# Kernel tuning notes

Measured on AMD Instinct MI355X. Metric: run time of the kernel, lower is better.

## Reference

```python
import jax, jax.numpy as jnp
import numpy as np

N_NODES = 100000
N_EDGES = 1000000
N_RELS = 8
N_HEADS = 4
IN_FEAT = 64
OUT_FEAT = 64
D_HEAD = OUT_FEAT // N_HEADS
LEAKY_SLOPE = 0.2


def setup_inputs() -> dict:
    key = jax.random.key(0)
    ks = jax.random.split(key, 8)
    x = jax.random.normal(ks[0], (N_NODES, IN_FEAT), dtype=jnp.float32)
    src_idx = jax.random.randint(ks[1], (N_EDGES,), 0, N_NODES)
    dst_idx = jax.random.randint(ks[2], (N_EDGES,), 0, N_NODES)
    edge_rel = jnp.sort(jax.random.randint(ks[3], (N_EDGES,), 0, N_RELS))
    # xavier-ish small init for weights
    conv_weights = jax.random.normal(ks[4], (N_RELS, N_HEADS, IN_FEAT, D_HEAD), dtype=jnp.float32) * 0.1
    attn_l = jax.random.normal(ks[5], (N_RELS, N_HEADS, D_HEAD), dtype=jnp.float32) * 0.1
    attn_r = jax.random.normal(ks[6], (N_RELS, N_HEADS, D_HEAD), dtype=jnp.float32) * 0.1
    h_bias = jnp.zeros((OUT_FEAT,), dtype=jnp.float32)
    return {
        'x': x, 'src_idx': src_idx, 'dst_idx': dst_idx, 'edge_rel': edge_rel,
        'conv_weights': conv_weights, 'attn_l': attn_l, 'attn_r': attn_r,
        'h_bias': h_bias,
    }


def reference(x, src_idx, dst_idx, edge_rel, conv_weights, attn_l, attn_r, h_bias):
    N = x.shape[0]
    # Per-relation transform of all node features: [R, N, H, D]
    feat_all = jnp.einsum('ni,rhid->rnhd', x, conv_weights)
    # Per-relation attention logits per node: [R, N, H]
    el_all = jnp.einsum('rnhd,rhd->rnh', feat_all, attn_l)
    er_all = jnp.einsum('rnhd,rhd->rnh', feat_all, attn_r)
    # Gather per-edge quantities (relation-specific transform of src/dst)
    feat_e = feat_all[edge_rel, src_idx]          # [E, H, D]
    el = el_all[edge_rel, src_idx]                # [E, H]
    er = er_all[edge_rel, dst_idx]                # [E, H]
    s = jax.nn.leaky_relu(el + er, negative_slope=LEAKY_SLOPE)
    # Edge softmax over incoming edges of each destination node (per head)
    m = jax.ops.segment_max(s, dst_idx, num_segments=N)      # [N, H]
    e = jnp.exp(s - m[dst_idx])                               # [E, H]
    denom = jax.ops.segment_sum(e, dst_idx, num_segments=N)   # [N, H]
    w = e / jnp.maximum(denom[dst_idx], jnp.float32(1e-16))   # [E, H]
    # Weighted aggregation of source features into destination nodes
    agg = jax.ops.segment_sum(feat_e * w[..., None], dst_idx, num_segments=N)  # [N, H, D]
    h = agg.reshape(N, OUT_FEAT) + h_bias
    # activation=None, dropout in eval mode -> identity
    return h
```

## Files before the change

### kernel.cpp

```cpp
#include <hip/hip_runtime.h>
#include <hip/hip_bf16.h>

#define NN 100000
#define NE 1000000
#define NR 8

#define EB 4096
#define NBLK 245
#define NBUCK 196
#define NT (NBUCK*NBLK)
#define NBB 188

typedef unsigned short u16;
typedef unsigned int u32;
typedef __attribute__((ext_vector_type(8))) short bf16x8;
typedef __attribute__((ext_vector_type(4))) float f32x4;

static __device__ __forceinline__ float bf2f(u16 u) {
    union { u32 i; float f; } v; v.i = ((u32)u) << 16; return v.f;
}
static __device__ __forceinline__ float bflo(u32 u) {
    union { u32 i; float f; } v; v.i = u << 16; return v.f;
}
static __device__ __forceinline__ float bfhi(u32 u) {
    union { u32 i; float f; } v; v.i = u & 0xffff0000u; return v.f;
}
static __device__ __forceinline__ u16 f2bf(float f) {
    __hip_bfloat16 h = __float2bfloat16(f);
    return *reinterpret_cast<u16*>(&h);
}
static __device__ __forceinline__ float ldf(const void* p, int idx, int isf32) {
    return isf32 ? ((const float*)p)[idx] : bf2f(((const u16*)p)[idx]);
}

__global__ void k_detect(const u16* __restrict__ xw, int* __restrict__ flag)
{
    int t = threadIdx.x;
    int insane = 0;
    for (int k = t; k < 512; k += 64) {
        u16 w = xw[k];
        int ex = (w >> 7) & 0xFF;
        bool sane = ((w & 0x7FFF) == 0) || (ex >= 96 && ex <= 159);
        insane += sane ? 0 : 1;
    }
    for (int off = 32; off; off >>= 1) insane += __shfl_down(insane, off);
    if (t == 0) *flag = (insane > 50) ? 1 : 0;
}

__global__ void k_cvt(const void* __restrict__ xin, const int* __restrict__ flag,
                      u16* __restrict__ xb)
{
    int i = blockIdx.x * blockDim.x + threadIdx.x;
    if (i >= NN * 8) return;
    if (*flag) {
        const float* xf = (const float*)xin;
        u16 o[8];
#pragma unroll
        for (int j = 0; j < 8; ++j) o[j] = f2bf(xf[i * 8 + j]);
        uint4 v;
        v.x = (u32)o[0] | ((u32)o[1] << 16);
        v.y = (u32)o[2] | ((u32)o[3] << 16);
        v.z = (u32)o[4] | ((u32)o[5] << 16);
        v.w = (u32)o[6] | ((u32)o[7] << 16);
        ((uint4*)xb)[i] = v;
    } else {
        ((uint4*)xb)[i] = ((const uint4*)xin)[i];
    }
}

__global__ void k0_prep(const void* __restrict__ cw, const void* __restrict__ al,
                        const void* __restrict__ ar, const int* __restrict__ flag,
                        u16* __restrict__ Bpre)
{
    int tid = blockIdx.x * blockDim.x + threadIdx.x;
    if (tid >= NR * 5120) return;
    int isf32 = *flag;
    int r = tid / 5120, rem = tid % 5120;
    int c = rem >> 3, j = rem & 7;
    int nt = c >> 7, kk = (c >> 6) & 1, lc = c & 63;
    int i = kk * 32 + ((lc >> 4) << 3) + j;
    int d = lc & 15;
    u16 val;
    if (nt < 4) {
        val = f2bf(ldf(cw, ((r * 4 + nt) * 64 + i) * 16 + d, isf32));
    } else if (d < 8) {
        int h = d >> 1;
        const void* attn = (d & 1) ? ar : al;
        float s = 0.f;
        for (int dd = 0; dd < 16; ++dd)
            s += ldf(cw, ((r * 4 + h) * 64 + i) * 16 + dd, isf32)
               * ldf(attn, (r * 4 + h) * 16 + dd, isf32);
        val = f2bf(s);
    } else {
        val = 0;
    }
    Bpre[tid] = val;
}

__global__ __launch_bounds__(256) void k1_feat(
    const u16* __restrict__ xb, const u16* __restrict__ Bpre,
    u16* __restrict__ feat_all, float* __restrict__ el_all, float* __restrict__ er_all)
{
    __shared__ alignas(16) u16 ldsA[4096];
    __shared__ alignas(16) u16 ldsB[5120];
    int n0 = blockIdx.x * 64;
    int r = blockIdx.y;
    int tid = threadIdx.x;
    int wave = tid >> 6, lane = tid & 63;

    for (int c = tid; c < 512; c += 256) {
        int mt = c >> 7, kk = (c >> 6) & 1, lc = c & 63;
        int node = n0 + mt * 16 + (lc & 15);
        if (node >= NN) node = NN - 1;
        int kbase = kk * 32 + ((lc >> 4) << 3);
        *(uint4*)&ldsA[c * 8] = *(const uint4*)&xb[node * 64 + kbase];
    }
    for (int c = tid; c < 640; c += 256)
        *(uint4*)&ldsB[c * 8] = *(const uint4*)&Bpre[r * 5120 + c * 8];
    __syncthreads();

    bf16x8 afrag0 = *(bf16x8*)&ldsA[((wave * 2 + 0) * 64 + lane) * 8];
    bf16x8 afrag1 = *(bf16x8*)&ldsA[((wave * 2 + 1) * 64 + lane) * 8];
    f32x4 acc[5];
#pragma unroll
    for (int nt = 0; nt < 5; ++nt) acc[nt] = f32x4{0.f, 0.f, 0.f, 0.f};
#pragma unroll
    for (int nt = 0; nt < 5; ++nt) {
        bf16x8 b0 = *(bf16x8*)&ldsB[((nt * 2 + 0) * 64 + lane) * 8];
        bf16x8 b1 = *(bf16x8*)&ldsB[((nt * 2 + 1) * 64 + lane) * 8];
        acc[nt] = __builtin_amdgcn_mfma_f32_16x16x32_bf16(afrag0, b0, acc[nt], 0, 0, 0);
        acc[nt] = __builtin_amdgcn_mfma_f32_16x16x32_bf16(afrag1, b1, acc[nt], 0, 0, 0);
    }

    int col = lane & 15, quad = lane >> 4;
    if (col < 8) {
        int h = col >> 1;
        float* dstp = (col & 1) ? er_all : el_all;
#pragma unroll
        for (int reg = 0; reg < 4; ++reg) {
            int node = n0 + wave * 16 + quad * 4 + reg;
            if (node < NN) dstp[(r * NN + node) * 4 + h] = acc[4][reg];
        }
    }
    __syncthreads();
#pragma unroll
    for (int nt = 0; nt < 4; ++nt) {
        int cg = nt * 16 + col;
#pragma unroll
        for (int reg = 0; reg < 4; ++reg) {
            int row = quad * 4 + reg;
            ldsA[(wave * 16 + row) * 64 + cg] = f2bf(acc[nt][reg]);
        }
    }
    __syncthreads();
    for (int c = tid; c < 512; c += 256) {
        int nl = c >> 3, part = c & 7;
        int node = n0 + nl;
        if (node < NN)
            *(uint4*)&feat_all[(r * NN + node) * 64 + part * 8] = *(uint4*)&ldsA[c * 8];
    }
}

__global__ __launch_bounds__(256) void k_binA(const int* __restrict__ dsti,
                                              int* __restrict__ histT)
{
    __shared__ int hist[NBUCK];
    int t = threadIdx.x, blk = blockIdx.x;
    if (t < NBUCK) hist[t] = 0;
    __syncthreads();
    int base = blk * EB;
    for (int j = 0; j < EB; j += 256) {
        int e = base + j + t;
        if (e < NE) atomicAdd(&hist[dsti[e] >> 9], 1);
    }
    __syncthreads();
    if (t < NBUCK) histT[t * NBLK + blk] = hist[t];
}

__global__ __launch_bounds__(256) void k_scanB1(int* __restrict__ histT,
                                                int* __restrict__ bsum)
{
    __shared__ int wtot[4];
    int t = threadIdx.x;
    int gi = blockIdx.x * 256 + t;
    int v = (gi < NT) ? histT[gi] : 0;
    int lane = t & 63, w = t >> 6;
    int s = v;
#pragma unroll
    for (int m = 1; m < 64; m <<= 1) {
        int u = __shfl_up(s, m);
        if (lane >= m) s += u;
    }
    if (lane == 63) wtot[w] = s;
    __syncthreads();
    int wb = 0;
    for (int i = 0; i < w; ++i) wb += wtot[i];
    if (gi < NT) histT[gi] = wb + s - v;
    if (t == 255) bsum[blockIdx.x] = wb + s;
}

__global__ __launch_bounds__(256) void k_scanB2(const int* __restrict__ bsum,
                                                int* __restrict__ boff)
{
    __shared__ int wtot[4];
    int t = threadIdx.x;
    int v = (t < NBB) ? bsum[t] : 0;
    int lane = t & 63, w = t >> 6;
    int s = v;
#pragma unroll
    for (int m = 1; m < 64; m <<= 1) {
        int u = __shfl_up(s, m);
        if (lane >= m) s += u;
    }
    if (lane == 63) wtot[w] = s;
    __syncthreads();
    int wb = 0;
    for (int i = 0; i < w; ++i) wb += wtot[i];
    if (t < NBB) boff[t] = wb + s - v;
}

__global__ __launch_bounds__(256) void k_scanB3(const int* __restrict__ boff,
                                                int* __restrict__ histT,
                                                int* __restrict__ bstart)
{
    int gi = blockIdx.x * 256 + threadIdx.x;
    if (gi < NT) {
        int val = histT[gi] + boff[blockIdx.x];
        histT[gi] = val;
        if (gi % NBLK == 0) bstart[gi / NBLK] = val;
    }
    if (gi == 0) bstart[NBUCK] = NE;
}

__global__ __launch_bounds__(256) void k_binC(
    const int* __restrict__ srci, const int* __restrict__ dsti,
    const int* __restrict__ reli, const int* __restrict__ histT,
    int* __restrict__ key_b)
{
    __shared__ int cur[NBUCK];
    int t = threadIdx.x, blk = blockIdx.x;
    if (t < NBUCK) cur[t] = histT[t * NBLK + blk];
    __syncthreads();
    int base = blk * EB;
    for (int j = 0; j < EB; j += 256) {
        int e = base + j + t;
        if (e < NE) {
            int d = dsti[e];
            int key = ((d & 511) << 20) | (reli[e] << 17) | srci[e];
            int pos = atomicAdd(&cur[d >> 9], 1);
            key_b[pos] = key;
        }
    }
}

__global__ __launch_bounds__(512) void k_binD(
    const int* __restrict__ bstart, const int* __restrict__ key_b,
    int* __restrict__ key_s, int* __restrict__ off)
{
    __shared__ int cnt[512];
    __shared__ int wtot[8];
    int t = threadIdx.x, b = blockIdx.x;
    int s0 = bstart[b], s1 = bstart[b + 1];
    cnt[t] = 0;
    __syncthreads();
    for (int j = s0 + t; j < s1; j += 512)
        atomicAdd(&cnt[(key_b[j] >> 20) & 511], 1);
    __syncthreads();
    int v = cnt[t];
    int lane = t & 63, w = t >> 6;
    int s = v;
#pragma unroll
    for (int m = 1; m < 64; m <<= 1) {
        int u = __shfl_up(s, m);
        if (lane >= m) s += u;
    }
    if (lane == 63) wtot[w] = s;
    __syncthreads();
    int wb = 0;
    for (int i = 0; i < w; ++i) wb += wtot[i];
    int excl = s0 + wb + s - v;
    int d = (b << 9) + t;
    if (d < NN) off[d] = excl;
    __syncthreads();
    cnt[t] = excl;
    if (b == 0 && t == 0) off[NN] = NE;
    __syncthreads();
    for (int j = s0 + t; j < s1; j += 512) {
        int key = key_b[j];
        int pos = atomicAdd(&cnt[(key >> 20) & 511], 1);
        key_s[pos] = key;
    }
}

__global__ __launch_bounds__(256) void k3_node(
    const int* __restrict__ off, const int* __restrict__ key_s,
    const float* __restrict__ el_all, const float* __restrict__ er_all,
    const u16* __restrict__ feat_all, const void* __restrict__ bias,
    const int* __restrict__ flag, void* __restrict__ out)
{
    __shared__ int   ldsK[4][64];
    __shared__ float ldsE[4][64][4];
    int wave = threadIdx.x >> 6, lane = threadIdx.x & 63;
    int eg = lane >> 4;
    int fl = lane & 15;
    int h  = fl >> 2;
    int gw = blockIdx.x * 4 + wave;
    int nw = gridDim.x * 4;
    int isf32 = *flag;
    float bv0 = ldf(bias, fl * 4 + 0, isf32);
    float bv1 = ldf(bias, fl * 4 + 1, isf32);
    float bv2 = ldf(bias, fl * 4 + 2, isf32);
    float bv3 = ldf(bias, fl * 4 + 3, isf32);

    for (int d = gw; d < NN; d += nw) {
        int start = off[d], end = off[d + 1];
        int deg = end - start;

        float acc0 = 0.f, acc1 = 0.f, acc2 = 0.f, acc3 = 0.f, accW = 0.f;
        for (int base = 0; base < deg; base += 64) {
            int cn = min(64, deg - base);
            if (lane < cn) {
                int key = key_s[start + base + lane];
                int rel = (key >> 17) & 7, src = key & 131071;
                int kk = rel * NN + src;
                f32x4 el = *(const f32x4*)&el_all[kk * 4];
                f32x4 er = *(const f32x4*)&er_all[(rel * NN + d) * 4];
                f32x4 ee;
#pragma unroll
                for (int q = 0; q < 4; ++q) {
                    float v = el[q] + er[q];
                    v = v > 0.f ? v : 0.2f * v;
                    ee[q] = __expf(v);
                }
                ldsK[wave][lane] = kk;
                *(f32x4*)&ldsE[wave][lane][0] = ee;
            } else {
                ldsK[wave][lane] = 0;
                *(f32x4*)&ldsE[wave][lane][0] = f32x4{0.f, 0.f, 0.f, 0.f};
            }
            int cnr = (cn + 3) & ~3;
            for (int e = 0; e < cnr; e += 4) {
                int   ke = ldsK[wave][e + eg];
                float w  = ldsE[wave][e + eg][h];
                uint2 u  = *(const uint2*)&feat_all[ke * 64 + fl * 4];
                acc0 += bflo(u.x) * w;
                acc1 += bfhi(u.x) * w;
                acc2 += bflo(u.y) * w;
                acc3 += bfhi(u.y) * w;
                accW += w;
            }
        }
#pragma unroll
        for (int m = 16; m < 64; m <<= 1) {
            acc0 += __shfl_xor(acc0, m);
            acc1 += __shfl_xor(acc1, m);
            acc2 += __shfl_xor(acc2, m);
            acc3 += __shfl_xor(acc3, m);
            accW += __shfl_xor(accW, m);
        }
        float invh = 1.f / fmaxf(accW, 1e-16f);
        if (eg == 0) {
            float o0 = acc0 * invh + bv0;
            float o1 = acc1 * invh + bv1;
            float o2 = acc2 * invh + bv2;
            float o3 = acc3 * invh + bv3;
            if (isf32) {
                ((f32x4*)out)[d * 16 + fl] = f32x4{o0, o1, o2, o3};
            } else {
                uint2 st;
                st.x = (u32)f2bf(o0) | ((u32)f2bf(o1) << 16);
                st.y = (u32)f2bf(o2) | ((u32)f2bf(o3) << 16);
                *(uint2*)&((u16*)out)[d * 64 + fl * 4] = st;
            }
        }
    }
}

extern "C" void kernel_launch(void* const* d_in, const int* in_sizes, int n_in,
                              void* d_out, int out_size, void* d_ws, size_t ws_size,
                              hipStream_t stream)
{
    const void* x   = d_in[0];
    const int* srci = (const int*)d_in[1];
    const int* dsti = (const int*)d_in[2];
    const int* reli = (const int*)d_in[3];
    const void* cw  = d_in[4];
    const void* al  = d_in[5];
    const void* ar  = d_in[6];
    const void* hb  = d_in[7];

    char* ws = (char*)d_ws;
    u16*   feat_all = (u16*)  (ws + 0);
    float* el_all   = (float*)(ws + 102400000);
    float* er_all   = (float*)(ws + 115200000);
    int*   key_s    = (int*)  (ws + 128000000);
    int*   key_b    = (int*)  (ws + 132000000);
    int*   off      = (int*)  (ws + 136000000);
    int*   histT    = (int*)  (ws + 136400064);
    int*   bsum     = (int*)  (ws + 136592192);
    int*   boff     = (int*)  (ws + 136592960);
    int*   bstart   = (int*)  (ws + 136593728);
    u16*   Bpre     = (u16*)  (ws + 136594560);
    u16*   xb       = (u16*)  (ws + 136676480);
    int*   flag     = (int*)  (ws + 149476480);

    k_detect<<<1, 64, 0, stream>>>((const u16*)x, flag);
    k_cvt<<<(NN * 8 + 255) / 256, 256, 0, stream>>>(x, flag, xb);
    k0_prep<<<(NR * 5120 + 255) / 256, 256, 0, stream>>>(cw, al, ar, flag, Bpre);
    k1_feat<<<dim3((NN + 63) / 64, NR), 256, 0, stream>>>(xb, Bpre, feat_all, el_all, er_all);
    k_binA<<<NBLK, 256, 0, stream>>>(dsti, histT);
    k_scanB1<<<NBB, 256, 0, stream>>>(histT, bsum);
    k_scanB2<<<1, 256, 0, stream>>>(bsum, boff);
    k_scanB3<<<NBB, 256, 0, stream>>>(boff, histT, bstart);
    k_binC<<<NBLK, 256, 0, stream>>>(srci, dsti, reli, histT, key_b);
    k_binD<<<NBUCK, 512, 0, stream>>>(bstart, key_b, key_s, off);
    k3_node<<<(NN + 3) / 4, 256, 0, stream>>>(off, key_s, el_all, er_all, feat_all,
                                              hb, flag, d_out);
}
```

Before: 231.3 us.

## Tile node aggregation by 64 destinations with LDS-staged er and edge weights

The node aggregation kernel now gives each block 64 consecutive destination nodes and each wave 16 of them. It stages er for all relations and the CSR offsets in LDS, then precomputes edge keys and exp-scores for up to 256 edges per wave before gathering, with an overflow path that reads from global memory. The gather loop unrolls four edges per step so several feature loads are in flight at once. Dtype detection is folded into the conversion and prep kernels, removing one launch at the cost of redundant per-block detection.

```diff
diff --git a/kernel.cpp b/kernel.cpp
--- a/kernel.cpp
+++ b/kernel.cpp
@@ -11,6 +11,8 @@
 #define NT (NBUCK*NBLK)
 #define NBB 188
 
+#define CAP 256
+
 typedef unsigned short u16;
 typedef unsigned int u32;
 typedef __attribute__((ext_vector_type(8))) short bf16x8;
@@ -33,26 +35,36 @@
     return isf32 ? ((const float*)p)[idx] : bf2f(((const u16*)p)[idx]);
 }
 
-__global__ void k_detect(const u16* __restrict__ xw, int* __restrict__ flag)
-{
-    int t = threadIdx.x;
+static __device__ __forceinline__ int detect_wave(const u16* xw, int lane)
+{
     int insane = 0;
-    for (int k = t; k < 512; k += 64) {
+    for (int k = lane; k < 512; k += 64) {
         u16 w = xw[k];
         int ex = (w >> 7) & 0xFF;
         bool sane = ((w & 0x7FFF) == 0) || (ex >= 96 && ex <= 159);
         insane += sane ? 0 : 1;
     }
     for (int off = 32; off; off >>= 1) insane += __shfl_down(insane, off);
-    if (t == 0) *flag = (insane > 50) ? 1 : 0;
-}
-
-__global__ void k_cvt(const void* __restrict__ xin, const int* __restrict__ flag,
-                      u16* __restrict__ xb)
-{
-    int i = blockIdx.x * blockDim.x + threadIdx.x;
+    return insane;
+}
+
+__global__ __launch_bounds__(256) void k_cvt(const void* __restrict__ xin,
+                                             u16* __restrict__ xb, int* __restrict__ flag)
+{
+    __shared__ int sflag;
+    int t = threadIdx.x;
+    if (t < 64) {
+        int insane = detect_wave((const u16*)xin, t);
+        if (t == 0) {
+            sflag = (insane > 50) ? 1 : 0;
+            if (blockIdx.x == 0) *flag = sflag;
+        }
+    }
+    __syncthreads();
+    int isf32 = sflag;
+    int i = blockIdx.x * 256 + t;
     if (i >= NN * 8) return;
-    if (*flag) {
+    if (isf32) {
         const float* xf = (const float*)xin;
         u16 o[8];
 #pragma unroll
@@ -68,13 +80,20 @@
     }
 }
 
-__global__ void k0_prep(const void* __restrict__ cw, const void* __restrict__ al,
-                        const void* __restrict__ ar, const int* __restrict__ flag,
-                        u16* __restrict__ Bpre)
-{
-    int tid = blockIdx.x * blockDim.x + threadIdx.x;
+__global__ __launch_bounds__(256) void k0_prep(const void* __restrict__ xin,
+                        const void* __restrict__ cw, const void* __restrict__ al,
+                        const void* __restrict__ ar, u16* __restrict__ Bpre)
+{
+    __shared__ int sflag;
+    int t = threadIdx.x;
+    if (t < 64) {
+        int insane = detect_wave((const u16*)xin, t);
+        if (t == 0) sflag = (insane > 50) ? 1 : 0;
+    }
+    __syncthreads();
+    int isf32 = sflag;
+    int tid = blockIdx.x * 256 + t;
     if (tid >= NR * 5120) return;
-    int isf32 = *flag;
     int r = tid / 5120, rem = tid % 5120;
     int c = rem >> 3, j = rem & 7;
     int nt = c >> 7, kk = (c >> 6) & 1, lc = c & 63;
@@ -298,58 +317,105 @@
     const u16* __restrict__ feat_all, const void* __restrict__ bias,
     const int* __restrict__ flag, void* __restrict__ out)
 {
-    __shared__ int   ldsK[4][64];
-    __shared__ float ldsE[4][64][4];
-    int wave = threadIdx.x >> 6, lane = threadIdx.x & 63;
+    __shared__ float ldsER[64][8][4];
+    __shared__ int   ldsOffs[65];
+    __shared__ int   ldsKey[4][CAP];
+    __shared__ float ldsEE[4][CAP][4];
+    int t = threadIdx.x;
+    int wave = t >> 6, lane = t & 63;
     int eg = lane >> 4;
     int fl = lane & 15;
     int h  = fl >> 2;
-    int gw = blockIdx.x * 4 + wave;
-    int nw = gridDim.x * 4;
+    int d0 = blockIdx.x * 64;
     int isf32 = *flag;
+
+#pragma unroll
+    for (int r = 0; r < 8; ++r) {
+        int dl = t >> 2, q = t & 3;
+        int dd = d0 + dl; if (dd >= NN) dd = NN - 1;
+        ldsER[dl][r][q] = er_all[(r * NN + dd) * 4 + q];
+    }
+    if (t < 65) ldsOffs[t] = off[min(d0 + t, NN)];
+    __syncthreads();
+
+    int dlo = wave * 16;
+    int estart = ldsOffs[dlo], eend = ldsOffs[dlo + 16];
+    int count = eend - estart;
+    int scount = min(count, CAP);
+
+    for (int j = lane; j < scount; j += 64) {
+        int key = key_s[estart + j];
+        int rel = (key >> 17) & 7, src = key & 131071;
+        int dl = (key >> 20) & 63;
+        int kk = rel * NN + src;
+        f32x4 el = *(const f32x4*)&el_all[kk * 4];
+        f32x4 er = *(const f32x4*)&ldsER[dl][rel][0];
+        f32x4 ee;
+#pragma unroll
+        for (int q = 0; q < 4; ++q) {
+            float v = el[q] + er[q];
+            v = v > 0.f ? v : 0.2f * v;
+            ee[q] = __expf(v);
+        }
+        ldsKey[wave][j] = kk;
+        *(f32x4*)&ldsEE[wave][j][0] = ee;
+    }
+
     float bv0 = ldf(bias, fl * 4 + 0, isf32);
     float bv1 = ldf(bias, fl * 4 + 1, isf32);
     float bv2 = ldf(bias, fl * 4 + 2, isf32);
     float bv3 = ldf(bias, fl * 4 + 3, isf32);
 
-    for (int d = gw; d < NN; d += nw) {
-        int start = off[d], end = off[d + 1];
-        int deg = end - start;
-
+    for (int nl = 0; nl < 16; ++nl) {
+        int d = d0 + dlo + nl;
+        if (d >= NN) break;
+        int s  = ldsOffs[dlo + nl] - estart;
+        int e1 = ldsOffs[dlo + nl + 1] - estart;
         float acc0 = 0.f, acc1 = 0.f, acc2 = 0.f, acc3 = 0.f, accW = 0.f;
-        for (int base = 0; base < deg; base += 64) {
-            int cn = min(64, deg - base);
-            if (lane < cn) {
-                int key = key_s[start + base + lane];
+
+        int e1c = min(e1, CAP);
+        for (int base = s; base < e1c; base += 16) {
+            int kk[4]; float w[4];
+#pragma unroll
+            for (int q = 0; q < 4; ++q) {
+                int idx = base + q * 4 + eg;
+                bool vld = idx < e1c;
+                kk[q] = vld ? ldsKey[wave][idx] : 0;
+                w[q]  = vld ? ldsEE[wave][idx][h] : 0.f;
+            }
+            uint2 u[4];
+#pragma unroll
+            for (int q = 0; q < 4; ++q)
+                u[q] = *(const uint2*)&feat_all[kk[q] * 64 + fl * 4];
+#pragma unroll
+            for (int q = 0; q < 4; ++q) {
+                acc0 += bflo(u[q].x) * w[q];
+                acc1 += bfhi(u[q].x) * w[q];
+                acc2 += bflo(u[q].y) * w[q];
+                acc3 += bfhi(u[q].y) * w[q];
+                accW += w[q];
+            }
+        }
+        for (int base = max(s, CAP); base < e1; base += 4) {
+            int idx = base + eg;
+            int kk0 = 0; float w0 = 0.f;
+            if (idx < e1) {
+                int key = key_s[estart + idx];
                 int rel = (key >> 17) & 7, src = key & 131071;
-                int kk = rel * NN + src;
-                f32x4 el = *(const f32x4*)&el_all[kk * 4];
-                f32x4 er = *(const f32x4*)&er_all[(rel * NN + d) * 4];
-                f32x4 ee;
-#pragma unroll
-                for (int q = 0; q < 4; ++q) {
-                    float v = el[q] + er[q];
-                    v = v > 0.f ? v : 0.2f * v;
-                    ee[q] = __expf(v);
-                }
-                ldsK[wave][lane] = kk;
-                *(f32x4*)&ldsE[wave][lane][0] = ee;
-            } else {
-                ldsK[wave][lane] = 0;
-                *(f32x4*)&ldsE[wave][lane][0] = f32x4{0.f, 0.f, 0.f, 0.f};
+                kk0 = rel * NN + src;
+                int dl = (key >> 20) & 63;
+                float v = el_all[kk0 * 4 + h] + ldsER[dl][rel][h];
+                v = v > 0.f ? v : 0.2f * v;
+                w0 = __expf(v);
             }
-            int cnr = (cn + 3) & ~3;
-            for (int e = 0; e < cnr; e += 4) {
-                int   ke = ldsK[wave][e + eg];
-                float w  = ldsE[wave][e + eg][h];
-                uint2 u  = *(const uint2*)&feat_all[ke * 64 + fl * 4];
-                acc0 += bflo(u.x) * w;
-                acc1 += bfhi(u.x) * w;
-                acc2 += bflo(u.y) * w;
-                acc3 += bfhi(u.y) * w;
-                accW += w;
-            }
-        }
+            uint2 u = *(const uint2*)&feat_all[kk0 * 64 + fl * 4];
+            acc0 += bflo(u.x) * w0;
+            acc1 += bfhi(u.x) * w0;
+            acc2 += bflo(u.y) * w0;
+            acc3 += bfhi(u.y) * w0;
+            accW += w0;
+        }
+
 #pragma unroll
         for (int m = 16; m < 64; m <<= 1) {
             acc0 += __shfl_xor(acc0, m);
@@ -404,9 +470,8 @@
     u16*   xb       = (u16*)  (ws + 136676480);
     int*   flag     = (int*)  (ws + 149476480);
 
-    k_detect<<<1, 64, 0, stream>>>((const u16*)x, flag);
-    k_cvt<<<(NN * 8 + 255) / 256, 256, 0, stream>>>(x, flag, xb);
-    k0_prep<<<(NR * 5120 + 255) / 256, 256, 0, stream>>>(cw, al, ar, flag, Bpre);
+    k_cvt<<<(NN * 8 + 255) / 256, 256, 0, stream>>>(x, xb, flag);
+    k0_prep<<<(NR * 5120 + 255) / 256, 256, 0, stream>>>(x, cw, al, ar, Bpre);
     k1_feat<<<dim3((NN + 63) / 64, NR), 256, 0, stream>>>(xb, Bpre, feat_all, el_all, er_all);
     k_binA<<<NBLK, 256, 0, stream>>>(dsti, histT);
     k_scanB1<<<NBB, 256, 0, stream>>>(histT, bsum);
@@ -414,6 +479,6 @@
     k_scanB3<<<NBB, 256, 0, stream>>>(boff, histT, bstart);
     k_binC<<<NBLK, 256, 0, stream>>>(srci, dsti, reli, histT, key_b);
     k_binD<<<NBUCK, 512, 0, stream>>>(bstart, key_b, key_s, off);
-    k3_node<<<(NN + 3) / 4, 256, 0, stream>>>(off, key_s, el_all, er_all, feat_all,
-                                              hb, flag, d_out);
-}
+    k3_node<<<(NN + 63) / 64, 256, 0, stream>>>(off, key_s, el_all, er_all, feat_all,
+                                                hb, flag, d_out);
+}
```

Result: no change. 229.9 us (-0.6%).
